# Kernel tuning notes

Hardware: AMD Instinct MI355X
Metric: run time of the kernel (lower is better)

## Reference

```python
import jax, jax.numpy as jnp
import numpy as np
from jax import lax

B, C, T = 64, 9, 8192
PCD, E, K = 16, 128, 7  # per_channel_dim, embed_dim, kernel_size
EPS = 1e-5


def setup_inputs() -> dict:
    key = jax.random.key(0)
    ks = jax.random.split(key, 5)
    fan_conv = 1.0 / np.sqrt(1 * K)
    fan_proj = 1.0 / np.sqrt(C * PCD)
    return {
        "x": jax.random.normal(ks[0], (B, C, T), dtype=jnp.float32),
        "w_conv": jax.random.uniform(ks[1], (C, PCD, K), jnp.float32, -fan_conv, fan_conv),
        "b_conv": jax.random.uniform(ks[2], (C, PCD), jnp.float32, -fan_conv, fan_conv),
        "w_proj": jax.random.uniform(ks[3], (E, C * PCD), jnp.float32, -fan_proj, fan_proj),
        "b_proj": jax.random.uniform(ks[4], (E,), jnp.float32, -fan_proj, fan_proj),
        "gamma": jnp.ones((E,), jnp.float32),
        "beta": jnp.zeros((E,), jnp.float32),
    }


def reference(x, w_conv, b_conv, w_proj, b_proj, gamma, beta):
    # 9 independent Conv1d(1 -> 16, k=7, pad=3) == grouped conv, groups=C.
    kernel = w_conv.reshape(C * PCD, 1, K)  # [144, 1, 7] (OIH)
    y = lax.conv_general_dilated(
        x, kernel, window_strides=(1,), padding=[(K // 2, K // 2)],
        dimension_numbers=("NCH", "OIH", "NCH"), feature_group_count=C,
    )  # [B, 144, T]
    y = jax.nn.relu(y + b_conv.reshape(C * PCD)[None, :, None])
    # 1x1 conv projection + permute(0,2,1): [B, T, E]
    z = jnp.einsum("bct,ec->bte", y, w_proj) + b_proj
    # LayerNorm over last dim (biased variance, eps=1e-5)
    mean = jnp.mean(z, axis=-1, keepdims=True)
    var = jnp.mean(jnp.square(z - mean), axis=-1, keepdims=True)
    return gamma * (z - mean) * lax.rsqrt(var + EPS) + beta
```

## Files before the change

kernel.cpp:

```cpp
#include <hip/hip_runtime.h>

#define B_    64
#define C_    9
#define T_    8192
#define PCD_  16
#define E_    128
#define K_    7
#define CP_   144
#define KPAD  160
#define TTILE 64
#define YSTR  168
#define EPS_  1e-5f

typedef __bf16 bf16x8 __attribute__((ext_vector_type(8)));
typedef float  f32x4  __attribute__((ext_vector_type(4)));

__global__ void prep_wb_kernel(const float* __restrict__ w_proj, __bf16* __restrict__ wb) {
    int idx = blockIdx.x * 256 + threadIdx.x;
    int row = idx / KPAD;
    int col = idx - row * KPAD;
    float v = (col < CP_) ? w_proj[row * CP_ + col] : 0.f;
    wb[idx] = (__bf16)v;
}

__global__ __launch_bounds__(256, 4)
void fused_kernel(const float* __restrict__ x, const float* __restrict__ w_conv,
                  const float* __restrict__ b_conv, const __bf16* __restrict__ wb,
                  const float* __restrict__ b_proj, const float* __restrict__ gamma,
                  const float* __restrict__ beta, float* __restrict__ out) {
    __shared__ __align__(16) float  x_lds[C_ * 72];
    __shared__ __align__(16) __bf16 y_lds[TTILE * YSTR];

    const int tid = threadIdx.x;
    const int bb = blockIdx.x >> 7;
    const int tt = blockIdx.x & 127;
    const int t0 = tt << 6;

    float wreg[K_];
    float bias = 0.f;
    if (tid < CP_) {
        #pragma unroll
        for (int k = 0; k < K_; ++k) wreg[k] = w_conv[tid * K_ + k];
        bias = b_conv[tid];
    }

    const float* xb = x + (size_t)bb * (C_ * T_);
    for (int o = tid; o < C_ * 70; o += 256) {
        int c = o / 70;
        int i = o - c * 70;
        int gt = t0 - 3 + i;
        x_lds[c * 72 + i] = (gt >= 0 && gt < T_) ? xb[c * T_ + gt] : 0.f;
    }
    for (int o = tid; o < TTILE * 8; o += 256) {
        int row = o >> 3, d = o & 7;
        *(unsigned int*)&y_lds[row * YSTR + CP_ + d * 2] = 0u;
    }
    __syncthreads();

    if (tid < CP_) {
        const int cp = tid;
        const int c  = cp >> 4;
        const float* xr = &x_lds[c * 72];
        #pragma unroll
        for (int tc = 0; tc < TTILE; tc += 8) {
            float xa[14];
            #pragma unroll
            for (int i = 0; i < 14; ++i) xa[i] = xr[tc + i];
            #pragma unroll
            for (int j = 0; j < 8; ++j) {
                float acc = bias;
                #pragma unroll
                for (int k = 0; k < K_; ++k) acc += xa[j + k] * wreg[k];
                y_lds[(tc + j) * YSTR + cp] = (__bf16)fmaxf(acc, 0.f);
            }
        }
    }
    __syncthreads();

    const int lane = tid & 63, wid = tid >> 6;
    const int n0 = wid * 16;
    const int fr = lane & 15, kg = lane >> 4;
    f32x4 acc[8];
    #pragma unroll
    for (int e = 0; e < 8; ++e) acc[e] = (f32x4){0.f, 0.f, 0.f, 0.f};

    #pragma unroll
    for (int ks = 0; ks < 5; ++ks) {
        const int k0 = ks * 32 + kg * 8;
        bf16x8 bfrag = *(const bf16x8*)&y_lds[(n0 + fr) * YSTR + k0];
        #pragma unroll
        for (int et = 0; et < 8; ++et) {
            bf16x8 afrag = *(const bf16x8*)&wb[(et * 16 + fr) * KPAD + k0];
            acc[et] = __builtin_amdgcn_mfma_f32_16x16x32_bf16(afrag, bfrag, acc[et], 0, 0, 0);
        }
    }

    const int t_local = n0 + fr;
    const int g = kg;
    float s = 0.f, ss = 0.f;
    #pragma unroll
    for (int et = 0; et < 8; ++et) {
        f32x4 bp = *(const f32x4*)&b_proj[et * 16 + g * 4];
        #pragma unroll
        for (int r = 0; r < 4; ++r) {
            float z = acc[et][r] + bp[r];
            acc[et][r] = z;
            s += z; ss += z * z;
        }
    }
    s  += __shfl_xor(s, 16);  s  += __shfl_xor(s, 32);
    ss += __shfl_xor(ss, 16); ss += __shfl_xor(ss, 32);
    const float mean = s * (1.f / 128.f);
    const float var  = ss * (1.f / 128.f) - mean * mean;
    const float rstd = rsqrtf(var + EPS_);

    float* orow = out + ((size_t)(bb * T_ + t0 + t_local)) * E_;
    #pragma unroll
    for (int et = 0; et < 8; ++et) {
        f32x4 gm = *(const f32x4*)&gamma[et * 16 + g * 4];
        f32x4 bt = *(const f32x4*)&beta[et * 16 + g * 4];
        f32x4 o4;
        #pragma unroll
        for (int r = 0; r < 4; ++r)
            o4[r] = (acc[et][r] - mean) * rstd * gm[r] + bt[r];
        *(f32x4*)&orow[et * 16 + g * 4] = o4;
    }
}

extern "C" void kernel_launch(void* const* d_in, const int* in_sizes, int n_in,
                              void* d_out, int out_size, void* d_ws, size_t ws_size,
                              hipStream_t stream) {
    const float* x      = (const float*)d_in[0];
    const float* w_conv = (const float*)d_in[1];
    const float* b_conv = (const float*)d_in[2];
    const float* w_proj = (const float*)d_in[3];
    const float* b_proj = (const float*)d_in[4];
    const float* gamma  = (const float*)d_in[5];
    const float* beta   = (const float*)d_in[6];
    float* out = (float*)d_out;
    __bf16* wb = (__bf16*)d_ws;

    hipLaunchKernelGGL(prep_wb_kernel, dim3(80), dim3(256), 0, stream, w_proj, wb);
    hipLaunchKernelGGL(fused_kernel, dim3(B_ * (T_ / TTILE)), dim3(256), 0, stream,
                       x, w_conv, b_conv, wb, b_proj, gamma, beta, out);
}
```

Measured before the change: 391.5 us.

## Loop multiple time tiles per block with double-buffered x prefetch

Each block now processes eight consecutive 64-step tiles instead of one, shrinking the grid eightfold. Idle threads prefetch the next tile's input into a second LDS buffer while the conv runs. Projection bias, gamma and beta are staged once in LDS. The aim is to amortize per-block setup and overlap input loads with compute. The cost is fewer resident blocks and serialized work with barriers per tile, which may reduce latency hiding for the output-store-bound workload.

New measurement: 378.1 us. -3.4%, faster.

```diff
diff --git a/kernel.cpp b/kernel.cpp
--- a/kernel.cpp
+++ b/kernel.cpp
@@ -9,6 +9,7 @@
 #define CP_   144
 #define KPAD  160
 #define TTILE 64
+#define NTILE 8
 #define YSTR  168
 #define EPS_  1e-5f
 
@@ -23,18 +24,19 @@
     wb[idx] = (__bf16)v;
 }
 
-__global__ __launch_bounds__(256, 4)
+__global__ __launch_bounds__(256)
 void fused_kernel(const float* __restrict__ x, const float* __restrict__ w_conv,
                   const float* __restrict__ b_conv, const __bf16* __restrict__ wb,
                   const float* __restrict__ b_proj, const float* __restrict__ gamma,
                   const float* __restrict__ beta, float* __restrict__ out) {
-    __shared__ __align__(16) float  x_lds[C_ * 72];
+    __shared__ __align__(16) float  xbuf[2][C_ * 72];
     __shared__ __align__(16) __bf16 y_lds[TTILE * YSTR];
+    __shared__ __align__(16) float  cba[3 * E_];
 
-    const int tid = threadIdx.x;
-    const int bb = blockIdx.x >> 7;
-    const int tt = blockIdx.x & 127;
-    const int t0 = tt << 6;
+    const int tid  = threadIdx.x;
+    const int bb   = blockIdx.x >> 4;
+    const int grp  = blockIdx.x & 15;
+    const int tbase = grp << 9;
 
     float wreg[K_];
     float bias = 0.f;
@@ -44,12 +46,15 @@
         bias = b_conv[tid];
     }
 
+    for (int o = tid; o < 3 * E_; o += 256) {
+        float v = (o < E_) ? b_proj[o] : (o < 2 * E_ ? gamma[o - E_] : beta[o - 2 * E_]);
+        cba[o] = v;
+    }
+
     const float* xb = x + (size_t)bb * (C_ * T_);
     for (int o = tid; o < C_ * 70; o += 256) {
-        int c = o / 70;
-        int i = o - c * 70;
-        int gt = t0 - 3 + i;
-        x_lds[c * 72 + i] = (gt >= 0 && gt < T_) ? xb[c * T_ + gt] : 0.f;
+        int c = o / 70, i = o - c * 70, gt = tbase - 3 + i;
+        xbuf[0][c * 72 + i] = (gt >= 0 && gt < T_) ? xb[c * T_ + gt] : 0.f;
     }
     for (int o = tid; o < TTILE * 8; o += 256) {
         int row = o >> 3, d = o & 7;
@@ -57,73 +62,101 @@
     }
     __syncthreads();
 
-    if (tid < CP_) {
-        const int cp = tid;
-        const int c  = cp >> 4;
-        const float* xr = &x_lds[c * 72];
-        #pragma unroll
-        for (int tc = 0; tc < TTILE; tc += 8) {
-            float xa[14];
+    const int lane = tid & 63;
+    const int wid  = tid >> 6;
+    const int n0 = wid * 16, fr = lane & 15, kg = lane >> 4;
+
+    for (int tile = 0; tile < NTILE; ++tile) {
+        const int t0  = tbase + (tile << 6);
+        const int cur = tile & 1;
+
+        if (tid < CP_) {
+            const int c = tid >> 4;
+            const float* xr = &xbuf[cur][c * 72];
             #pragma unroll
-            for (int i = 0; i < 14; ++i) xa[i] = xr[tc + i];
+            for (int tc = 0; tc < TTILE; tc += 8) {
+                float xa[14];
+                #pragma unroll
+                for (int i = 0; i < 14; ++i) xa[i] = xr[tc + i];
+                #pragma unroll
+                for (int j = 0; j < 8; ++j) {
+                    float acc = bias;
+                    #pragma unroll
+                    for (int k = 0; k < K_; ++k) acc += xa[j + k] * wreg[k];
+                    y_lds[(tc + j) * YSTR + tid] = (__bf16)fmaxf(acc, 0.f);
+                }
+            }
+        } else if (tid >= 192 && tile < NTILE - 1) {
+            const int t0n = t0 + TTILE;
+            const int so  = tid - 192;
+            float v[10];
             #pragma unroll
-            for (int j = 0; j < 8; ++j) {
-                float acc = bias;
-                #pragma unroll
-                for (int k = 0; k < K_; ++k) acc += xa[j + k] * wreg[k];
-                y_lds[(tc + j) * YSTR + cp] = (__bf16)fmaxf(acc, 0.f);
+            for (int j = 0; j < 10; ++j) {
+                int o = so + j * 64;
+                v[j] = 0.f;
+                if (o < C_ * 70) {
+                    int c = o / 70, i = o - c * 70, gt = t0n - 3 + i;
+                    if (gt >= 0 && gt < T_) v[j] = xb[c * T_ + gt];
+                }
+            }
+            #pragma unroll
+            for (int j = 0; j < 10; ++j) {
+                int o = so + j * 64;
+                if (o < C_ * 70) {
+                    int c = o / 70, i = o - c * 70;
+                    xbuf[cur ^ 1][c * 72 + i] = v[j];
+                }
             }
         }
-    }
-    __syncthreads();
+        __syncthreads();
 
-    const int lane = tid & 63, wid = tid >> 6;
-    const int n0 = wid * 16;
-    const int fr = lane & 15, kg = lane >> 4;
-    f32x4 acc[8];
-    #pragma unroll
-    for (int e = 0; e < 8; ++e) acc[e] = (f32x4){0.f, 0.f, 0.f, 0.f};
+        f32x4 acc[8];
+        #pragma unroll
+        for (int e = 0; e < 8; ++e) acc[e] = (f32x4){0.f, 0.f, 0.f, 0.f};
 
-    #pragma unroll
-    for (int ks = 0; ks < 5; ++ks) {
-        const int k0 = ks * 32 + kg * 8;
-        bf16x8 bfrag = *(const bf16x8*)&y_lds[(n0 + fr) * YSTR + k0];
+        #pragma unroll
+        for (int ks = 0; ks < 5; ++ks) {
+            const int k0 = ks * 32 + kg * 8;
+            bf16x8 bfrag = *(const bf16x8*)&y_lds[(n0 + fr) * YSTR + k0];
+            #pragma unroll
+            for (int et = 0; et < 8; ++et) {
+                bf16x8 afrag = *(const bf16x8*)&wb[(et * 16 + fr) * KPAD + k0];
+                acc[et] = __builtin_amdgcn_mfma_f32_16x16x32_bf16(afrag, bfrag, acc[et], 0, 0, 0);
+            }
+        }
+
+        const int t_local = n0 + fr;
+        const int g = kg;
+        float s = 0.f, ss = 0.f;
         #pragma unroll
         for (int et = 0; et < 8; ++et) {
-            bf16x8 afrag = *(const bf16x8*)&wb[(et * 16 + fr) * KPAD + k0];
-            acc[et] = __builtin_amdgcn_mfma_f32_16x16x32_bf16(afrag, bfrag, acc[et], 0, 0, 0);
+            f32x4 bp = *(const f32x4*)&cba[et * 16 + g * 4];
+            #pragma unroll
+            for (int r = 0; r < 4; ++r) {
+                float z = acc[et][r] + bp[r];
+                acc[et][r] = z;
+                s += z; ss += z * z;
+            }
         }
-    }
+        s  += __shfl_xor(s, 16);  s  += __shfl_xor(s, 32);
+        ss += __shfl_xor(ss, 16); ss += __shfl_xor(ss, 32);
+        const float mean = s * (1.f / 128.f);
+        const float var  = ss * (1.f / 128.f) - mean * mean;
+        const float rstd = rsqrtf(var + EPS_);
 
-    const int t_local = n0 + fr;
-    const int g = kg;
-    float s = 0.f, ss = 0.f;
-    #pragma unroll
-    for (int et = 0; et < 8; ++et) {
-        f32x4 bp = *(const f32x4*)&b_proj[et * 16 + g * 4];
+        float* orow = out + ((size_t)(bb * T_ + t0 + t_local)) * E_;
         #pragma unroll
-        for (int r = 0; r < 4; ++r) {
-            float z = acc[et][r] + bp[r];
-            acc[et][r] = z;
-            s += z; ss += z * z;
+        for (int et = 0; et < 8; ++et) {
+            f32x4 gm = *(const f32x4*)&cba[E_ + et * 16 + g * 4];
+            f32x4 bt = *(const f32x4*)&cba[2 * E_ + et * 16 + g * 4];
+            f32x4 o4;
+            #pragma unroll
+            for (int r = 0; r < 4; ++r)
+                o4[r] = (acc[et][r] - mean) * rstd * gm[r] + bt[r];
+            *(f32x4*)&orow[et * 16 + g * 4] = o4;
         }
-    }
-    s  += __shfl_xor(s, 16);  s  += __shfl_xor(s, 32);
-    ss += __shfl_xor(ss, 16); ss += __shfl_xor(ss, 32);
-    const float mean = s * (1.f / 128.f);
-    const float var  = ss * (1.f / 128.f) - mean * mean;
-    const float rstd = rsqrtf(var + EPS_);
 
-    float* orow = out + ((size_t)(bb * T_ + t0 + t_local)) * E_;
-    #pragma unroll
-    for (int et = 0; et < 8; ++et) {
-        f32x4 gm = *(const f32x4*)&gamma[et * 16 + g * 4];
-        f32x4 bt = *(const f32x4*)&beta[et * 16 + g * 4];
-        f32x4 o4;
-        #pragma unroll
-        for (int r = 0; r < 4; ++r)
-            o4[r] = (acc[et][r] - mean) * rstd * gm[r] + bt[r];
-        *(f32x4*)&orow[et * 16 + g * 4] = o4;
+        if (tile < NTILE - 1) __syncthreads();
     }
 }
 
@@ -141,6 +174,6 @@
     __bf16* wb = (__bf16*)d_ws;
 
     hipLaunchKernelGGL(prep_wb_kernel, dim3(80), dim3(256), 0, stream, w_proj, wb);
-    hipLaunchKernelGGL(fused_kernel, dim3(B_ * (T_ / TTILE)), dim3(256), 0, stream,
+    hipLaunchKernelGGL(fused_kernel, dim3(B_ * 16), dim3(256), 0, stream,
                        x, w_conv, b_conv, wb, b_proj, gamma, beta, out);
 }
```
